# Kernel optimization log

Hardware: AMD Instinct MI355X
Metric: run time of the kernel (lower is better)

Reference implementation:

```python
import jax, jax.numpy as jnp
import numpy as np

M = 8192          # tokens
DIM = 2048        # per-stream width; K = 4*DIM
S = 4             # fixed stream count (Stream4 kernels)
N = 32            # fixed GEMM output width
SINKHORN_ITERS = 20


def setup_inputs() -> dict:
    key = jax.random.key(0)
    k1, k2 = jax.random.split(key)
    X = jax.random.normal(k1, (M, S * DIM), dtype=jnp.float32)
    # scale W so H = X @ W is O(1): keeps sigmoid/exp/sinkhorn numerically sane
    W = jax.random.normal(k2, (S * DIM, N), dtype=jnp.float32) / np.float32(np.sqrt(S * DIM))
    # module init: beta = zeros(24), alpha = ones(3), concatenated
    alpha_beta = jnp.concatenate([jnp.zeros(24, jnp.float32), jnp.ones(3, jnp.float32)])
    return {"X": X, "W": W, "alpha_beta": alpha_beta}


def _sinkhorn(P, iters=SINKHORN_ITERS):
    # doubly-stochastic normalization of [M, S, S] matrices
    for _ in range(iters):
        P = P / jnp.sum(P, axis=-1, keepdims=True)  # row normalize
        P = P / jnp.sum(P, axis=-2, keepdims=True)  # col normalize
    return P


def reference(X, W, alpha_beta):
    Mm, K = X.shape
    d = K // S
    # skinny GEMM producing the mixing logits (fused w/ SplitK in the kernel)
    H = X @ W                                   # [M, 32]
    b_res, b_pre, b_pos = alpha_beta[0:16], alpha_beta[16:20], alpha_beta[20:24]
    a_res, a_pre, a_pos = alpha_beta[24], alpha_beta[25], alpha_beta[26]
    H_pre = a_pre * jax.nn.sigmoid(H[:, 16:20]) + b_pre          # [M, 4]
    H_pos = a_pos * jax.nn.sigmoid(H[:, 20:24]) + b_pos          # [M, 4]
    H_res = (a_res * H[:, 0:16] + b_res).reshape(Mm, S, S)       # [M, 4, 4]
    H_res = _sinkhorn(jnp.exp(H_res))                            # doubly stochastic
    # view X as 4 streams of width d
    Xs = X.reshape(Mm, S, d)                                     # [M, 4, d]
    # ApplyPreTransform: collapse streams with H_pre weights
    Y = jnp.einsum('ms,msd->md', H_pre, Xs)                      # [M, d]
    # ApplyResidual: per-token 4x4 stream mix + broadcast of pre-transformed feature
    O = jnp.einsum('msi,mid->msd', H_res, Xs) + H_pos[:, :, None] * Y[:, None, :]
    return O.reshape(Mm, K)
```

## Files before the change

### kernel.cpp

```cpp
#include <hip/hip_runtime.h>
#include <math.h>
#include <stdint.h>

#define K_DIM 8192
#define D_DIM 2048
#define M_ROWS 8192
#define N_W 32
#define NC 24
#define RB 4
#define THREADS 512
#define TOTAL_KSTEPS (K_DIM / 32)

typedef short bf16x8 __attribute__((ext_vector_type(8)));
typedef float f32x4 __attribute__((ext_vector_type(4)));
union U32x4 { uint32_t u[4]; bf16x8 v; };

#define WFRAG_IDX(ks, tile, hilo) ((((ks) * 2 + (tile)) * 2 + (hilo)) * 64)

__global__ __launch_bounds__(256) void mhc_prepack_kernel(
    const float* __restrict__ W, unsigned short* __restrict__ wfrag)
{
    const int idx = blockIdx.x * 256 + threadIdx.x;
    const int k = idx >> 5, n = idx & 31;
    const float w = W[(size_t)k * N_W + n];
    const uint32_t u = __float_as_uint(w);
    const float hif = __uint_as_float(u & 0xFFFF0000u);
    const uint32_t ur = __float_as_uint(w - hif);

    const int ks = k >> 5, kk = k & 31;
    const int lane = ((kk >> 3) << 4) | (n & 15);
    const int e = kk & 7;
    const int tile = n >> 4;
    unsigned short* p = wfrag + ((size_t)WFRAG_IDX(ks, tile, 0) + lane) * 8 + e;
    p[0]   = (unsigned short)(u >> 16);
    p[512] = (unsigned short)(ur >> 16);
}

__global__ __launch_bounds__(THREADS, 4) void mhc_fused_kernel(
    const float* __restrict__ X, const unsigned short* __restrict__ wfrag,
    const float* __restrict__ ab, float* __restrict__ out)
{
    __shared__ __align__(16) float Xl[RB * D_DIM];
    __shared__ float Hpart[8][RB][NC];
    __shared__ float pbuf[RB][NC];

    const int t = threadIdx.x;
    const int l = t & 63;
    const int wv = t >> 6;
    const int rowbase = blockIdx.x * RB;

    const float4* __restrict__ Xg = reinterpret_cast<const float4*>(X);
    float4 x4[RB][4];
#pragma unroll
    for (int i = 0; i < 4; ++i)
#pragma unroll
        for (int r = 0; r < RB; ++r)
            x4[r][i] = Xg[(size_t)(rowbase + r) * (K_DIM / 4) + i * 512 + t];

    f32x4 c0 = {0.f, 0.f, 0.f, 0.f};
    f32x4 c1 = {0.f, 0.f, 0.f, 0.f};
    const bf16x8* __restrict__ wf = reinterpret_cast<const bf16x8*>(wfrag);
    const int abase = (l & 3) * D_DIM + ((l >> 4) << 3);

#pragma unroll
    for (int i = 0; i < 4; ++i) {
        if (i) __syncthreads();
#pragma unroll
        for (int r = 0; r < RB; ++r)
            *reinterpret_cast<float4*>(&Xl[r * D_DIM + (t << 2)]) = x4[r][i];
        __syncthreads();

#pragma unroll
        for (int s = 0; s < 8; ++s) {
            const int ksl = wv * 8 + s;
            const int ks = i * 64 + ksl;
            const float* xp = &Xl[abase + ksl * 32];
            const float4 xa = *reinterpret_cast<const float4*>(xp);
            const float4 xb = *reinterpret_cast<const float4*>(xp + 4);
            float xs[8];
            xs[0] = xa.x; xs[1] = xa.y; xs[2] = xa.z; xs[3] = xa.w;
            xs[4] = xb.x; xs[5] = xb.y; xs[6] = xb.z; xs[7] = xb.w;

            U32x4 ah, al;
#pragma unroll
            for (int p = 0; p < 4; ++p) {
                const uint32_t u0 = __float_as_uint(xs[2 * p]);
                const uint32_t u1 = __float_as_uint(xs[2 * p + 1]);
                const float h0 = __uint_as_float(u0 & 0xFFFF0000u);
                const float h1 = __uint_as_float(u1 & 0xFFFF0000u);
                const uint32_t r0 = __float_as_uint(xs[2 * p] - h0);
                const uint32_t r1 = __float_as_uint(xs[2 * p + 1] - h1);
                ah.u[p] = (u1 & 0xFFFF0000u) | (u0 >> 16);
                al.u[p] = (r1 & 0xFFFF0000u) | (r0 >> 16);
            }

            const bf16x8 bh0 = wf[WFRAG_IDX(ks, 0, 0) + l];
            const bf16x8 bl0 = wf[WFRAG_IDX(ks, 0, 1) + l];
            const bf16x8 bh1 = wf[WFRAG_IDX(ks, 1, 0) + l];
            const bf16x8 bl1 = wf[WFRAG_IDX(ks, 1, 1) + l];

            c0 = __builtin_amdgcn_mfma_f32_16x16x32_bf16(ah.v, bh0, c0, 0, 0, 0);
            c0 = __builtin_amdgcn_mfma_f32_16x16x32_bf16(al.v, bh0, c0, 0, 0, 0);
            c0 = __builtin_amdgcn_mfma_f32_16x16x32_bf16(ah.v, bl0, c0, 0, 0, 0);
            c1 = __builtin_amdgcn_mfma_f32_16x16x32_bf16(ah.v, bh1, c1, 0, 0, 0);
            c1 = __builtin_amdgcn_mfma_f32_16x16x32_bf16(al.v, bh1, c1, 0, 0, 0);
            c1 = __builtin_amdgcn_mfma_f32_16x16x32_bf16(ah.v, bl1, c1, 0, 0, 0);
        }
    }

    __syncthreads();
    if (l < 16) {
#pragma unroll
        for (int r = 0; r < RB; ++r) Hpart[wv][r][l] = c0[r];
    }
    if (l < 8) {
#pragma unroll
        for (int r = 0; r < RB; ++r) Hpart[wv][r][16 + l] = c1[r];
    }
    __syncthreads();

    if (wv == 0) {
        float h0 = 0.f;
#pragma unroll
        for (int w = 0; w < 8; ++w) h0 += Hpart[w][l >> 4][l & 15];
        float p = __expf(fmaf(ab[24], h0, ab[l & 15]));

        if (l < 32) {
            float h1 = 0.f;
#pragma unroll
            for (int w = 0; w < 8; ++w) h1 += Hpart[w][l >> 3][16 + (l & 7)];
            const int ci = 16 + (l & 7);
            const float sc = (ci < 20) ? ab[25] : ab[26];
            pbuf[l >> 3][ci] = fmaf(sc, 1.f / (1.f + __expf(-h1)), ab[ci]);
        }

        for (int it = 0; it < 20; ++it) {
            float rs = p + __shfl_xor(p, 1);
            rs += __shfl_xor(rs, 2);
            p = p / rs;
            float cs = p + __shfl_xor(p, 4);
            cs += __shfl_xor(cs, 8);
            p = p / cs;
        }
        pbuf[l >> 4][l & 15] = p;
    }
    __syncthreads();

    float4* __restrict__ Og = reinterpret_cast<float4*>(out);
#pragma unroll
    for (int r = 0; r < RB; ++r) {
        float hre[4][4], hpr[4], hpo[4];
#pragma unroll
        for (int q = 0; q < 16; ++q) hre[q >> 2][q & 3] = pbuf[r][q];
#pragma unroll
        for (int q = 0; q < 4; ++q) hpr[q] = pbuf[r][16 + q];
#pragma unroll
        for (int q = 0; q < 4; ++q) hpo[q] = pbuf[r][20 + q];

        float y[4];
#pragma unroll
        for (int e = 0; e < 4; ++e) {
            float v = 0.f;
#pragma unroll
            for (int i = 0; i < 4; ++i)
                v = fmaf(hpr[i], reinterpret_cast<const float*>(&x4[r][i])[e], v);
            y[e] = v;
        }

        const size_t ob = (size_t)(rowbase + r) * (K_DIM / 4);
#pragma unroll
        for (int s = 0; s < 4; ++s) {
            float4 o;
            float* oe = reinterpret_cast<float*>(&o);
#pragma unroll
            for (int e = 0; e < 4; ++e) {
                float v = hpo[s] * y[e];
#pragma unroll
                for (int i = 0; i < 4; ++i)
                    v = fmaf(hre[s][i],
                             reinterpret_cast<const float*>(&x4[r][i])[e], v);
                oe[e] = v;
            }
            Og[ob + s * 512 + t] = o;
        }
    }
}

extern "C" void kernel_launch(void* const* d_in, const int* in_sizes, int n_in,
                              void* d_out, int out_size, void* d_ws, size_t ws_size,
                              hipStream_t stream) {
    const float* X  = (const float*)d_in[0];
    const float* W  = (const float*)d_in[1];
    const float* ab = (const float*)d_in[2];
    float* out = (float*)d_out;
    unsigned short* wfrag = (unsigned short*)d_ws;

    mhc_prepack_kernel<<<(K_DIM * N_W) / 256, 256, 0, stream>>>(W, wfrag);
    mhc_fused_kernel<<<M_ROWS / RB, THREADS, 0, stream>>>(X, wfrag, ab, out);
}
```

Before: 182.4 us.

## Replace split-bf16 MFMA GEMM with per-thread FP32 FMA and cross-lane reduction

Drops the shared-memory staging of X and the three-term bf16 hi/lo MFMA emulation. Each thread now accumulates its own 4x24 partial dot products in FP32 registers from its loaded X slice and a W prepacked to match that thread's K indices, then reduces with wave shuffles and a shared-memory cross-wave sum. The prepack now only keeps the 24 used columns. This removes LDS traffic, barriers and bit-split conversions and gives exact FP32, but adds 96 accumulator registers per thread (occupancy hint lowered to 2) and a long 96x6 shuffle reduction.

```diff
diff --git a/kernel.cpp b/kernel.cpp
--- a/kernel.cpp
+++ b/kernel.cpp
@@ -3,135 +3,108 @@
 #include <stdint.h>
 
 #define K_DIM 8192
-#define D_DIM 2048
 #define M_ROWS 8192
-#define N_W 32
 #define NC 24
 #define RB 4
-#define THREADS 512
-#define TOTAL_KSTEPS (K_DIM / 32)
+#define T 512
 
-typedef short bf16x8 __attribute__((ext_vector_type(8)));
 typedef float f32x4 __attribute__((ext_vector_type(4)));
-union U32x4 { uint32_t u[4]; bf16x8 v; };
-
-#define WFRAG_IDX(ks, tile, hilo) ((((ks) * 2 + (tile)) * 2 + (hilo)) * 64)
 
 __global__ __launch_bounds__(256) void mhc_prepack_kernel(
-    const float* __restrict__ W, unsigned short* __restrict__ wfrag)
+    const float* __restrict__ W, f32x4* __restrict__ Wp)
 {
     const int idx = blockIdx.x * 256 + threadIdx.x;
-    const int k = idx >> 5, n = idx & 31;
-    const float w = W[(size_t)k * N_W + n];
-    const uint32_t u = __float_as_uint(w);
-    const float hif = __uint_as_float(u & 0xFFFF0000u);
-    const uint32_t ur = __float_as_uint(w - hif);
-
-    const int ks = k >> 5, kk = k & 31;
-    const int lane = ((kk >> 3) << 4) | (n & 15);
-    const int e = kk & 7;
-    const int tile = n >> 4;
-    unsigned short* p = wfrag + ((size_t)WFRAG_IDX(ks, tile, 0) + lane) * 8 + e;
-    p[0]   = (unsigned short)(u >> 16);
-    p[512] = (unsigned short)(ur >> 16);
+    const int t = idx & 511;
+    const int g = idx >> 9;
+    const int u = g % 6;
+    const int e = (g / 6) & 3;
+    const int c = g / 24;
+    const int k = c * 2048 + 4 * t + e;
+    const float* wr = W + (size_t)k * 32 + 4 * u;
+    f32x4 v = {wr[0], wr[1], wr[2], wr[3]};
+    Wp[idx] = v;
 }
 
-__global__ __launch_bounds__(THREADS, 4) void mhc_fused_kernel(
-    const float* __restrict__ X, const unsigned short* __restrict__ wfrag,
+__global__ __launch_bounds__(T, 2) void mhc_fused_kernel(
+    const float* __restrict__ X, const f32x4* __restrict__ Wp,
     const float* __restrict__ ab, float* __restrict__ out)
 {
-    __shared__ __align__(16) float Xl[RB * D_DIM];
-    __shared__ float Hpart[8][RB][NC];
+    __shared__ float red[8][96];
+    __shared__ float Hf[96];
     __shared__ float pbuf[RB][NC];
 
     const int t = threadIdx.x;
     const int l = t & 63;
     const int wv = t >> 6;
-    const int rowbase = blockIdx.x * RB;
+    const size_t rowbase = (size_t)blockIdx.x * RB;
 
-    const float4* __restrict__ Xg = reinterpret_cast<const float4*>(X);
-    float4 x4[RB][4];
+    const f32x4* __restrict__ Xg = reinterpret_cast<const f32x4*>(X);
+
+    f32x4 x4[RB][4];
 #pragma unroll
-    for (int i = 0; i < 4; ++i)
+    for (int c = 0; c < 4; ++c)
 #pragma unroll
         for (int r = 0; r < RB; ++r)
-            x4[r][i] = Xg[(size_t)(rowbase + r) * (K_DIM / 4) + i * 512 + t];
+            x4[r][c] = Xg[(rowbase + r) * 2048 + c * 512 + t];
 
-    f32x4 c0 = {0.f, 0.f, 0.f, 0.f};
-    f32x4 c1 = {0.f, 0.f, 0.f, 0.f};
-    const bf16x8* __restrict__ wf = reinterpret_cast<const bf16x8*>(wfrag);
-    const int abase = (l & 3) * D_DIM + ((l >> 4) << 3);
+    float acc[RB][NC];
+#pragma unroll
+    for (int r = 0; r < RB; ++r)
+#pragma unroll
+        for (int n = 0; n < NC; ++n) acc[r][n] = 0.f;
 
 #pragma unroll
-    for (int i = 0; i < 4; ++i) {
-        if (i) __syncthreads();
+    for (int c = 0; c < 4; ++c) {
 #pragma unroll
-        for (int r = 0; r < RB; ++r)
-            *reinterpret_cast<float4*>(&Xl[r * D_DIM + (t << 2)]) = x4[r][i];
-        __syncthreads();
-
+        for (int e = 0; e < 4; ++e) {
 #pragma unroll
-        for (int s = 0; s < 8; ++s) {
-            const int ksl = wv * 8 + s;
-            const int ks = i * 64 + ksl;
-            const float* xp = &Xl[abase + ksl * 32];
-            const float4 xa = *reinterpret_cast<const float4*>(xp);
-            const float4 xb = *reinterpret_cast<const float4*>(xp + 4);
-            float xs[8];
-            xs[0] = xa.x; xs[1] = xa.y; xs[2] = xa.z; xs[3] = xa.w;
-            xs[4] = xb.x; xs[5] = xb.y; xs[6] = xb.z; xs[7] = xb.w;
-
-            U32x4 ah, al;
+            for (int u = 0; u < 6; ++u) {
+                const f32x4 w = Wp[(size_t)((c * 4 + e) * 6 + u) * 512 + t];
 #pragma unroll
-            for (int p = 0; p < 4; ++p) {
-                const uint32_t u0 = __float_as_uint(xs[2 * p]);
-                const uint32_t u1 = __float_as_uint(xs[2 * p + 1]);
-                const float h0 = __uint_as_float(u0 & 0xFFFF0000u);
-                const float h1 = __uint_as_float(u1 & 0xFFFF0000u);
-                const uint32_t r0 = __float_as_uint(xs[2 * p] - h0);
-                const uint32_t r1 = __float_as_uint(xs[2 * p + 1] - h1);
-                ah.u[p] = (u1 & 0xFFFF0000u) | (u0 >> 16);
-                al.u[p] = (r1 & 0xFFFF0000u) | (r0 >> 16);
+                for (int r = 0; r < RB; ++r) {
+                    const float xv = x4[r][c][e];
+                    acc[r][u * 4 + 0] = fmaf(xv, w[0], acc[r][u * 4 + 0]);
+                    acc[r][u * 4 + 1] = fmaf(xv, w[1], acc[r][u * 4 + 1]);
+                    acc[r][u * 4 + 2] = fmaf(xv, w[2], acc[r][u * 4 + 2]);
+                    acc[r][u * 4 + 3] = fmaf(xv, w[3], acc[r][u * 4 + 3]);
+                }
             }
-
-            const bf16x8 bh0 = wf[WFRAG_IDX(ks, 0, 0) + l];
-            const bf16x8 bl0 = wf[WFRAG_IDX(ks, 0, 1) + l];
-            const bf16x8 bh1 = wf[WFRAG_IDX(ks, 1, 0) + l];
-            const bf16x8 bl1 = wf[WFRAG_IDX(ks, 1, 1) + l];
-
-            c0 = __builtin_amdgcn_mfma_f32_16x16x32_bf16(ah.v, bh0, c0, 0, 0, 0);
-            c0 = __builtin_amdgcn_mfma_f32_16x16x32_bf16(al.v, bh0, c0, 0, 0, 0);
-            c0 = __builtin_amdgcn_mfma_f32_16x16x32_bf16(ah.v, bl0, c0, 0, 0, 0);
-            c1 = __builtin_amdgcn_mfma_f32_16x16x32_bf16(ah.v, bh1, c1, 0, 0, 0);
-            c1 = __builtin_amdgcn_mfma_f32_16x16x32_bf16(al.v, bh1, c1, 0, 0, 0);
-            c1 = __builtin_amdgcn_mfma_f32_16x16x32_bf16(ah.v, bl1, c1, 0, 0, 0);
         }
     }
 
+    float v1 = 0.f, v2 = 0.f;
+#pragma unroll
+    for (int fl = 0; fl < 96; ++fl) {
+        float v = acc[fl / NC][fl % NC];
+        v += __shfl_xor(v, 1);
+        v += __shfl_xor(v, 2);
+        v += __shfl_xor(v, 4);
+        v += __shfl_xor(v, 8);
+        v += __shfl_xor(v, 16);
+        v += __shfl_xor(v, 32);
+        if (l == fl) v1 = v;
+        if (l == fl - 64) v2 = v;
+    }
+    red[wv][l] = v1;
+    if (l < 32) red[wv][64 + l] = v2;
     __syncthreads();
-    if (l < 16) {
+
+    if (t < 96) {
+        float h = 0.f;
 #pragma unroll
-        for (int r = 0; r < RB; ++r) Hpart[wv][r][l] = c0[r];
-    }
-    if (l < 8) {
-#pragma unroll
-        for (int r = 0; r < RB; ++r) Hpart[wv][r][16 + l] = c1[r];
+        for (int w = 0; w < 8; ++w) h += red[w][t];
+        Hf[t] = h;
     }
     __syncthreads();
 
     if (wv == 0) {
-        float h0 = 0.f;
-#pragma unroll
-        for (int w = 0; w < 8; ++w) h0 += Hpart[w][l >> 4][l & 15];
-        float p = __expf(fmaf(ab[24], h0, ab[l & 15]));
+        const int row = l >> 4, idx = l & 15;
+        float p = __expf(fmaf(ab[24], Hf[row * NC + idx], ab[idx]));
 
         if (l < 32) {
-            float h1 = 0.f;
-#pragma unroll
-            for (int w = 0; w < 8; ++w) h1 += Hpart[w][l >> 3][16 + (l & 7)];
-            const int ci = 16 + (l & 7);
+            const int rr = l >> 3, ci = 16 + (l & 7);
             const float sc = (ci < 20) ? ab[25] : ab[26];
-            pbuf[l >> 3][ci] = fmaf(sc, 1.f / (1.f + __expf(-h1)), ab[ci]);
+            pbuf[rr][ci] = fmaf(sc, 1.f / (1.f + __expf(-Hf[rr * NC + ci])), ab[ci]);
         }
 
         for (int it = 0; it < 20; ++it) {
@@ -142,11 +115,17 @@
             cs += __shfl_xor(cs, 8);
             p = p / cs;
         }
-        pbuf[l >> 4][l & 15] = p;
+        pbuf[row][idx] = p;
     }
     __syncthreads();
 
-    float4* __restrict__ Og = reinterpret_cast<float4*>(out);
+#pragma unroll
+    for (int r = 0; r < RB; ++r)
+#pragma unroll
+        for (int c = 0; c < 4; ++c)
+            asm volatile("" : "+v"(x4[r][c]));
+
+    f32x4* __restrict__ Og = reinterpret_cast<f32x4*>(out);
 #pragma unroll
     for (int r = 0; r < RB; ++r) {
         float hre[4][4], hpr[4], hpo[4];
@@ -157,31 +136,15 @@
 #pragma unroll
         for (int q = 0; q < 4; ++q) hpo[q] = pbuf[r][20 + q];
 
-        float y[4];
-#pragma unroll
-        for (int e = 0; e < 4; ++e) {
-            float v = 0.f;
-#pragma unroll
-            for (int i = 0; i < 4; ++i)
-                v = fmaf(hpr[i], reinterpret_cast<const float*>(&x4[r][i])[e], v);
-            y[e] = v;
-        }
+        f32x4 y = hpr[0] * x4[r][0] + hpr[1] * x4[r][1] +
+                  hpr[2] * x4[r][2] + hpr[3] * x4[r][3];
 
-        const size_t ob = (size_t)(rowbase + r) * (K_DIM / 4);
 #pragma unroll
         for (int s = 0; s < 4; ++s) {
-            float4 o;
-            float* oe = reinterpret_cast<float*>(&o);
-#pragma unroll
-            for (int e = 0; e < 4; ++e) {
-                float v = hpo[s] * y[e];
-#pragma unroll
-                for (int i = 0; i < 4; ++i)
-                    v = fmaf(hre[s][i],
-                             reinterpret_cast<const float*>(&x4[r][i])[e], v);
-                oe[e] = v;
-            }
-            Og[ob + s * 512 + t] = o;
+            f32x4 o = hpo[s] * y
+                    + hre[s][0] * x4[r][0] + hre[s][1] * x4[r][1]
+                    + hre[s][2] * x4[r][2] + hre[s][3] * x4[r][3];
+            Og[(rowbase + r) * 2048 + s * 512 + t] = o;
         }
     }
 }
@@ -193,8 +156,8 @@
     const float* W  = (const float*)d_in[1];
     const float* ab = (const float*)d_in[2];
     float* out = (float*)d_out;
-    unsigned short* wfrag = (unsigned short*)d_ws;
+    f32x4* Wp = (f32x4*)d_ws;
 
-    mhc_prepack_kernel<<<(K_DIM * N_W) / 256, 256, 0, stream>>>(W, wfrag);
-    mhc_fused_kernel<<<M_ROWS / RB, THREADS, 0, stream>>>(X, wfrag, ab, out);
+    mhc_prepack_kernel<<<192, 256, 0, stream>>>(W, Wp);
+    mhc_fused_kernel<<<M_ROWS / RB, T, 0, stream>>>(X, Wp, ab, out);
 }
```

Measured after the change: 269.1 us. +47.5%, slower.

## Use full 16-row MFMA tiles, load X fragments directly, drop W low split

Applied to the files above, without the earlier changes.

Each block now handles 16 rows so every MFMA tile row is used, where before only 4 of 16 were. X fragments go straight from global memory into registers with a software-pipelined prefetch over each wave's K slice, which removes the LDS staging and its barriers. W is rounded to a single bf16 instead of a hi/lo pair, cutting MFMAs per step from 6 to 4. The epilogue re-reads X from global memory, so X is fetched twice, and the coarser W rounding lowers GEMM accuracy.

```diff
diff --git a/kernel.cpp b/kernel.cpp
--- a/kernel.cpp
+++ b/kernel.cpp
@@ -7,15 +7,17 @@
 #define M_ROWS 8192
 #define N_W 32
 #define NC 24
-#define RB 4
+#define ROWS 16
 #define THREADS 512
-#define TOTAL_KSTEPS (K_DIM / 32)
+#define WAVES 8
+#define KPW 32
+#define OUTER 8
 
 typedef short bf16x8 __attribute__((ext_vector_type(8)));
 typedef float f32x4 __attribute__((ext_vector_type(4)));
 union U32x4 { uint32_t u[4]; bf16x8 v; };
 
-#define WFRAG_IDX(ks, tile, hilo) ((((ks) * 2 + (tile)) * 2 + (hilo)) * 64)
+#define WFI(ks, tile) (((ks) * 2 + (tile)) * 64)
 
 __global__ __launch_bounds__(256) void mhc_prepack_kernel(
     const float* __restrict__ W, unsigned short* __restrict__ wfrag)
@@ -24,59 +26,64 @@
     const int k = idx >> 5, n = idx & 31;
     const float w = W[(size_t)k * N_W + n];
     const uint32_t u = __float_as_uint(w);
-    const float hif = __uint_as_float(u & 0xFFFF0000u);
-    const uint32_t ur = __float_as_uint(w - hif);
+    const uint32_t r = u + 0x7FFFu + ((u >> 16) & 1u);
 
     const int ks = k >> 5, kk = k & 31;
     const int lane = ((kk >> 3) << 4) | (n & 15);
     const int e = kk & 7;
     const int tile = n >> 4;
-    unsigned short* p = wfrag + ((size_t)WFRAG_IDX(ks, tile, 0) + lane) * 8 + e;
-    p[0]   = (unsigned short)(u >> 16);
-    p[512] = (unsigned short)(ur >> 16);
+    wfrag[((size_t)WFI(ks, tile) + lane) * 8 + e] = (unsigned short)(r >> 16);
 }
 
 __global__ __launch_bounds__(THREADS, 4) void mhc_fused_kernel(
     const float* __restrict__ X, const unsigned short* __restrict__ wfrag,
     const float* __restrict__ ab, float* __restrict__ out)
 {
-    __shared__ __align__(16) float Xl[RB * D_DIM];
-    __shared__ float Hpart[8][RB][NC];
-    __shared__ float pbuf[RB][NC];
+    __shared__ float Hpart[WAVES][ROWS][NC];
+    __shared__ float Hf[ROWS * NC];
+    __shared__ float pbuf[ROWS * NC];
 
     const int t = threadIdx.x;
     const int l = t & 63;
     const int wv = t >> 6;
-    const int rowbase = blockIdx.x * RB;
+    const int rowbase = blockIdx.x * ROWS;
 
     const float4* __restrict__ Xg = reinterpret_cast<const float4*>(X);
-    float4 x4[RB][4];
-#pragma unroll
-    for (int i = 0; i < 4; ++i)
-#pragma unroll
-        for (int r = 0; r < RB; ++r)
-            x4[r][i] = Xg[(size_t)(rowbase + r) * (K_DIM / 4) + i * 512 + t];
+    const bf16x8* __restrict__ wf = reinterpret_cast<const bf16x8*>(wfrag);
+
+    const int ks0 = wv * KPW;
+    const int arow = rowbase + (l & 15);
+    const size_t xbase = (size_t)arow * (K_DIM / 4) + ((l >> 4) << 1);
 
     f32x4 c0 = {0.f, 0.f, 0.f, 0.f};
     f32x4 c1 = {0.f, 0.f, 0.f, 0.f};
-    const bf16x8* __restrict__ wf = reinterpret_cast<const bf16x8*>(wfrag);
-    const int abase = (l & 3) * D_DIM + ((l >> 4) << 3);
-
-#pragma unroll
-    for (int i = 0; i < 4; ++i) {
-        if (i) __syncthreads();
-#pragma unroll
-        for (int r = 0; r < RB; ++r)
-            *reinterpret_cast<float4*>(&Xl[r * D_DIM + (t << 2)]) = x4[r][i];
-        __syncthreads();
-
-#pragma unroll
-        for (int s = 0; s < 8; ++s) {
-            const int ksl = wv * 8 + s;
-            const int ks = i * 64 + ksl;
-            const float* xp = &Xl[abase + ksl * 32];
-            const float4 xa = *reinterpret_cast<const float4*>(xp);
-            const float4 xb = *reinterpret_cast<const float4*>(xp + 4);
+
+    float4 px[4][2];
+    bf16x8 pb[4][2];
+#pragma unroll
+    for (int s = 0; s < 4; ++s) {
+        px[s][0] = Xg[xbase + (size_t)(ks0 + s) * 8];
+        px[s][1] = Xg[xbase + (size_t)(ks0 + s) * 8 + 1];
+        pb[s][0] = wf[WFI(ks0 + s, 0) + l];
+        pb[s][1] = wf[WFI(ks0 + s, 1) + l];
+    }
+
+    for (int c = 0; c < OUTER; ++c) {
+#pragma unroll
+        for (int s = 0; s < 4; ++s) {
+            const float4 xa = px[s][0];
+            const float4 xb = px[s][1];
+            const bf16x8 b0 = pb[s][0];
+            const bf16x8 b1 = pb[s][1];
+
+            if (c + 1 < OUTER) {
+                const int ks = ks0 + (c + 1) * 4 + s;
+                px[s][0] = Xg[xbase + (size_t)ks * 8];
+                px[s][1] = Xg[xbase + (size_t)ks * 8 + 1];
+                pb[s][0] = wf[WFI(ks, 0) + l];
+                pb[s][1] = wf[WFI(ks, 1) + l];
+            }
+
             float xs[8];
             xs[0] = xa.x; xs[1] = xa.y; xs[2] = xa.z; xs[3] = xa.w;
             xs[4] = xb.x; xs[5] = xb.y; xs[6] = xb.z; xs[7] = xb.w;
@@ -94,44 +101,43 @@
                 al.u[p] = (r1 & 0xFFFF0000u) | (r0 >> 16);
             }
 
-            const bf16x8 bh0 = wf[WFRAG_IDX(ks, 0, 0) + l];
-            const bf16x8 bl0 = wf[WFRAG_IDX(ks, 0, 1) + l];
-            const bf16x8 bh1 = wf[WFRAG_IDX(ks, 1, 0) + l];
-            const bf16x8 bl1 = wf[WFRAG_IDX(ks, 1, 1) + l];
-
-            c0 = __builtin_amdgcn_mfma_f32_16x16x32_bf16(ah.v, bh0, c0, 0, 0, 0);
-            c0 = __builtin_amdgcn_mfma_f32_16x16x32_bf16(al.v, bh0, c0, 0, 0, 0);
-            c0 = __builtin_amdgcn_mfma_f32_16x16x32_bf16(ah.v, bl0, c0, 0, 0, 0);
-            c1 = __builtin_amdgcn_mfma_f32_16x16x32_bf16(ah.v, bh1, c1, 0, 0, 0);
-            c1 = __builtin_amdgcn_mfma_f32_16x16x32_bf16(al.v, bh1, c1, 0, 0, 0);
-            c1 = __builtin_amdgcn_mfma_f32_16x16x32_bf16(ah.v, bl1, c1, 0, 0, 0);
-        }
-    }
-
+            c0 = __builtin_amdgcn_mfma_f32_16x16x32_bf16(ah.v, b0, c0, 0, 0, 0);
+            c0 = __builtin_amdgcn_mfma_f32_16x16x32_bf16(al.v, b0, c0, 0, 0, 0);
+            c1 = __builtin_amdgcn_mfma_f32_16x16x32_bf16(ah.v, b1, c1, 0, 0, 0);
+            c1 = __builtin_amdgcn_mfma_f32_16x16x32_bf16(al.v, b1, c1, 0, 0, 0);
+        }
+    }
+
+#pragma unroll
+    for (int r = 0; r < 4; ++r)
+        Hpart[wv][((l >> 4) << 2) + r][l & 15] = c0[r];
+    if ((l & 15) < 8) {
+#pragma unroll
+        for (int r = 0; r < 4; ++r)
+            Hpart[wv][((l >> 4) << 2) + r][16 + (l & 15)] = c1[r];
+    }
     __syncthreads();
-    if (l < 16) {
-#pragma unroll
-        for (int r = 0; r < RB; ++r) Hpart[wv][r][l] = c0[r];
-    }
-    if (l < 8) {
-#pragma unroll
-        for (int r = 0; r < RB; ++r) Hpart[wv][r][16 + l] = c1[r];
+
+    if (t < ROWS * NC) {
+        float h = 0.f;
+#pragma unroll
+        for (int w = 0; w < WAVES; ++w)
+            h += Hpart[w][t / NC][t % NC];
+        Hf[t] = h;
     }
     __syncthreads();
 
-    if (wv == 0) {
-        float h0 = 0.f;
-#pragma unroll
-        for (int w = 0; w < 8; ++w) h0 += Hpart[w][l >> 4][l & 15];
-        float p = __expf(fmaf(ab[24], h0, ab[l & 15]));
+    if (wv < 4) {
+        const int row16 = wv * 4 + (l >> 4);
+        const int idx = l & 15;
+        float p = __expf(fmaf(ab[24], Hf[row16 * NC + idx], ab[idx]));
 
         if (l < 32) {
-            float h1 = 0.f;
-#pragma unroll
-            for (int w = 0; w < 8; ++w) h1 += Hpart[w][l >> 3][16 + (l & 7)];
+            const int rr = wv * 4 + (l >> 3);
             const int ci = 16 + (l & 7);
             const float sc = (ci < 20) ? ab[25] : ab[26];
-            pbuf[l >> 3][ci] = fmaf(sc, 1.f / (1.f + __expf(-h1)), ab[ci]);
+            pbuf[rr * NC + ci] =
+                fmaf(sc, 1.f / (1.f + __expf(-Hf[rr * NC + ci])), ab[ci]);
         }
 
         for (int it = 0; it < 20; ++it) {
@@ -142,20 +148,25 @@
             cs += __shfl_xor(cs, 8);
             p = p / cs;
         }
-        pbuf[l >> 4][l & 15] = p;
+        pbuf[row16 * NC + idx] = p;
     }
     __syncthreads();
 
     float4* __restrict__ Og = reinterpret_cast<float4*>(out);
-#pragma unroll
-    for (int r = 0; r < RB; ++r) {
+    for (int r = 0; r < ROWS; ++r) {
+        const float* pr = &pbuf[r * NC];
         float hre[4][4], hpr[4], hpo[4];
 #pragma unroll
-        for (int q = 0; q < 16; ++q) hre[q >> 2][q & 3] = pbuf[r][q];
-#pragma unroll
-        for (int q = 0; q < 4; ++q) hpr[q] = pbuf[r][16 + q];
-#pragma unroll
-        for (int q = 0; q < 4; ++q) hpo[q] = pbuf[r][20 + q];
+        for (int q = 0; q < 16; ++q) hre[q >> 2][q & 3] = pr[q];
+#pragma unroll
+        for (int q = 0; q < 4; ++q) hpr[q] = pr[16 + q];
+#pragma unroll
+        for (int q = 0; q < 4; ++q) hpo[q] = pr[20 + q];
+
+        const size_t rb4 = (size_t)(rowbase + r) * (K_DIM / 4);
+        float4 xq[4];
+#pragma unroll
+        for (int i = 0; i < 4; ++i) xq[i] = Xg[rb4 + i * 512 + t];
 
         float y[4];
 #pragma unroll
@@ -163,11 +174,10 @@
             float v = 0.f;
 #pragma unroll
             for (int i = 0; i < 4; ++i)
-                v = fmaf(hpr[i], reinterpret_cast<const float*>(&x4[r][i])[e], v);
+                v = fmaf(hpr[i], reinterpret_cast<const float*>(&xq[i])[e], v);
             y[e] = v;
         }
 
-        const size_t ob = (size_t)(rowbase + r) * (K_DIM / 4);
 #pragma unroll
         for (int s = 0; s < 4; ++s) {
             float4 o;
@@ -178,10 +188,10 @@
 #pragma unroll
                 for (int i = 0; i < 4; ++i)
                     v = fmaf(hre[s][i],
-                             reinterpret_cast<const float*>(&x4[r][i])[e], v);
+                             reinterpret_cast<const float*>(&xq[i])[e], v);
                 oe[e] = v;
             }
-            Og[ob + s * 512 + t] = o;
+            Og[rb4 + s * 512 + t] = o;
         }
     }
 }
@@ -196,5 +206,5 @@
     unsigned short* wfrag = (unsigned short*)d_ws;
 
     mhc_prepack_kernel<<<(K_DIM * N_W) / 256, 256, 0, stream>>>(W, wfrag);
-    mhc_fused_kernel<<<M_ROWS / RB, THREADS, 0, stream>>>(X, wfrag, ab, out);
+    mhc_fused_kernel<<<M_ROWS / ROWS, THREADS, 0, stream>>>(X, wfrag, ab, out);
 }
```

Result: faster. 167.1 us (-8.4%).
